# Performance work log

Measured on AMD Instinct MI355X. Metric: run time of the kernel, lower is better.

Reference implementation:

```python
import jax, jax.numpy as jnp
import numpy as np

DIM = 512
HEADS = 8
D_HEAD = 64
INNER_FF = 4 * DIM  # 2048
EPS = 1e-5
SCALE = D_HEAD ** -0.5


def _layernorm(x, w, b):
    x = x.astype(jnp.float32)
    mu = jnp.mean(x, axis=-1, keepdims=True)
    var = jnp.mean(jnp.square(x - mu), axis=-1, keepdims=True)
    return (x - mu) * jax.lax.rsqrt(var + EPS) * w + b


def _l2_attn(x, wq, bq, wv, bv, wo, bo):
    # x: [B, N, DIM]. k = q (context is ignored in the original module).
    b, n, _ = x.shape
    q = (x @ wq + bq).reshape(b, n, HEADS, D_HEAD).transpose(0, 2, 1, 3)  # b h n d
    v = (x @ wv + bv).reshape(b, n, HEADS, D_HEAD).transpose(0, 2, 1, 3)
    q = q.astype(jnp.float32)
    AB = jnp.einsum('bhid,bhjd->bhij', q, q)          # [b,h,n,n]
    AA = jnp.sum(jnp.square(q), axis=-1)               # [b,h,n]
    sim = -(AA[..., :, None] - 2.0 * AB + AA[..., None, :]) * SCALE
    attn = jax.nn.softmax(sim, axis=-1)
    out = jnp.einsum('bhij,bhjd->bhid', attn, v)       # [b,h,n,d]
    out = out.transpose(0, 2, 1, 3).reshape(b, n, HEADS * D_HEAD)
    return out @ wo + bo


def _geglu_ff(x, w1, b1, w2, b2):
    h = x @ w1 + b1                      # [B, N, 2*INNER_FF]
    a, gate = jnp.split(h, 2, axis=-1)
    return (a * jax.nn.gelu(gate, approximate=False)) @ w2 + b2


def setup_inputs() -> dict:
    key = jax.random.key(0)
    ks = jax.random.split(key, 24)
    s = 0.02
    d = {'x': jax.random.normal(ks[0], (4, 2048, DIM), jnp.float32)}
    # layernorms
    d['sa_norm_w'] = jnp.ones((DIM,), jnp.float32)
    d['sa_norm_b'] = jnp.zeros((DIM,), jnp.float32)
    d['ca_norm_w'] = jnp.ones((DIM,), jnp.float32)
    d['ca_norm_b'] = jnp.zeros((DIM,), jnp.float32)
    d['ff_norm_w'] = jnp.ones((DIM,), jnp.float32)
    d['ff_norm_b'] = jnp.zeros((DIM,), jnp.float32)
    # attn1 (self)
    d['a1_wq'] = jax.random.normal(ks[1], (DIM, DIM), jnp.float32) * s
    d['a1_bq'] = jnp.zeros((DIM,), jnp.float32)
    d['a1_wv'] = jax.random.normal(ks[2], (DIM, DIM), jnp.float32) * s
    d['a1_bv'] = jnp.zeros((DIM,), jnp.float32)
    d['a1_wo'] = jax.random.normal(ks[3], (DIM, DIM), jnp.float32) * s
    d['a1_bo'] = jnp.zeros((DIM,), jnp.float32)
    # attn2 (cross, but k=q and v from x in original code)
    d['a2_wq'] = jax.random.normal(ks[4], (DIM, DIM), jnp.float32) * s
    d['a2_bq'] = jnp.zeros((DIM,), jnp.float32)
    d['a2_wv'] = jax.random.normal(ks[5], (DIM, DIM), jnp.float32) * s
    d['a2_bv'] = jnp.zeros((DIM,), jnp.float32)
    d['a2_wo'] = jax.random.normal(ks[6], (DIM, DIM), jnp.float32) * s
    d['a2_bo'] = jnp.zeros((DIM,), jnp.float32)
    # GEGLU FFN
    d['ff_w1'] = jax.random.normal(ks[7], (DIM, 2 * INNER_FF), jnp.float32) * s
    d['ff_b1'] = jnp.zeros((2 * INNER_FF,), jnp.float32)
    d['ff_w2'] = jax.random.normal(ks[8], (INNER_FF, DIM), jnp.float32) * s
    d['ff_b2'] = jnp.zeros((DIM,), jnp.float32)
    return d


def reference(x, sa_norm_w, sa_norm_b, ca_norm_w, ca_norm_b, ff_norm_w, ff_norm_b,
              a1_wq, a1_bq, a1_wv, a1_bv, a1_wo, a1_bo,
              a2_wq, a2_bq, a2_wv, a2_bv, a2_wo, a2_bo,
              ff_w1, ff_b1, ff_w2, ff_b2):
    x = _l2_attn(_layernorm(x, sa_norm_w, sa_norm_b), a1_wq, a1_bq, a1_wv, a1_bv, a1_wo, a1_bo) + x
    x = _l2_attn(_layernorm(x, ca_norm_w, ca_norm_b), a2_wq, a2_bq, a2_wv, a2_bv, a2_wo, a2_bo) + x
    x = _geglu_ff(_layernorm(x, ff_norm_w, ff_norm_b), ff_w1, ff_b1, ff_w2, ff_b2) + x
    return x
```

## Files before the change

kernel.cpp:

```cpp
#include <hip/hip_runtime.h>
#include <hip/hip_bf16.h>


typedef short bf16x8 __attribute__((ext_vector_type(8)));
typedef float f32x4 __attribute__((ext_vector_type(4)));
typedef unsigned short u16;
typedef unsigned int u32;

__device__ __forceinline__ float bf2f(u16 u) {
    return __uint_as_float(((u32)u) << 16);
}
__device__ __forceinline__ u16 f2bf(float f) {
    u32 u = __float_as_uint(f);
    u32 rb = ((u >> 16) & 1u) + 0x7fffu;
    return (u16)((u + rb) >> 16);
}
__device__ __forceinline__ float gelu_fast(float x) {
    float y = 1.5957691216f * (x + 0.044715f * x * x * x);
    return x / (1.f + __expf(-y));
}
__device__ __forceinline__ void gl2lds16(const u16* g, u16* l) {
    __builtin_amdgcn_global_load_lds(
        (const __attribute__((address_space(1))) void*)(unsigned long long)(uintptr_t)g,
        (__attribute__((address_space(3))) void*)(unsigned long long)(uintptr_t)l,
        16, 0, 0);
}

struct TArgs {
    const float* src[8];
    u16* dst[8];
    int R[8], C[8];
    int start[9];
};
__global__ __launch_bounds__(256) void transpose_multi(TArgs a) {
    __shared__ float tile[32][33];
    int bid = blockIdx.x;
    int s = 0;
    while (bid >= a.start[s + 1]) s++;
    int local = bid - a.start[s];
    int R = a.R[s], C = a.C[s];
    int tx = C >> 5;
    int bx = local % tx, by = local / tx;
    const float* in = a.src[s];
    u16* out = a.dst[s];
    int t = threadIdx.x;
    int c = t & 31, r0 = (t >> 5) * 4;
#pragma unroll
    for (int i = 0; i < 4; i++)
        tile[r0 + i][c] = in[(size_t)(by * 32 + r0 + i) * C + bx * 32 + c];
    __syncthreads();
#pragma unroll
    for (int i = 0; i < 4; i++)
        out[(size_t)(bx * 32 + r0 + i) * R + by * 32 + c] = f2bf(tile[c][r0 + i]);
}

__global__ __launch_bounds__(256) void ln_kernel(const float* __restrict__ x,
                                                 const float* __restrict__ w,
                                                 const float* __restrict__ b,
                                                 u16* __restrict__ out) {
    int row = blockIdx.x, t = threadIdx.x;
    const float* xr = x + (size_t)row * 512;
    float2 v = *(const float2*)(xr + t * 2);
    float s1 = v.x + v.y;
    float s2 = v.x * v.x + v.y * v.y;
#pragma unroll
    for (int m = 1; m < 64; m <<= 1) {
        s1 += __shfl_xor(s1, m);
        s2 += __shfl_xor(s2, m);
    }
    __shared__ float r1[4], r2[4];
    int wave = t >> 6, lane = t & 63;
    if (lane == 0) { r1[wave] = s1; r2[wave] = s2; }
    __syncthreads();
    float tot1 = r1[0] + r1[1] + r1[2] + r1[3];
    float tot2 = r2[0] + r2[1] + r2[2] + r2[3];
    float mu = tot1 * (1.f / 512.f);
    float var = tot2 * (1.f / 512.f) - mu * mu;
    float rs = rsqrtf(var + 1e-5f);
    float2 wv = *(const float2*)(w + t * 2);
    float2 bv = *(const float2*)(b + t * 2);
    float o0 = (v.x - mu) * rs * wv.x + bv.x;
    float o1 = (v.y - mu) * rs * wv.y + bv.y;
    u32 pack = (u32)f2bf(o0) | ((u32)f2bf(o1) << 16);
    *(u32*)(out + (size_t)row * 512 + t * 2) = pack;
}

__global__ __launch_bounds__(256) void gemm_ff1(const u16* __restrict__ A,
                                                const u16* __restrict__ BT,
                                                const float* __restrict__ bias,
                                                u16* __restrict__ gout,
                                                int K) {
    __shared__ u16 As[2][128 * 32];
    __shared__ u16 Bs[2][128 * 32];
    int t = threadIdx.x;
    int wave = t >> 6, lane = t & 63, quad = lane >> 4, l16 = lane & 15;
    int m0 = blockIdx.x * 128, n0 = blockIdx.y * 64;
    f32x4 aacc[2][4], gacc[2][4];
#pragma unroll
    for (int i = 0; i < 2; i++)
#pragma unroll
        for (int j = 0; j < 4; j++) {
            aacc[i][j] = (f32x4){0.f, 0.f, 0.f, 0.f};
            gacc[i][j] = (f32x4){0.f, 0.f, 0.f, 0.f};
        }
    const u16* Ag = A + (size_t)(m0 + wave * 32 + (lane >> 2)) * K + (lane & 3) * 8;
    int brow = (wave < 2) ? (n0 + wave * 32) : (2048 + n0 + (wave - 2) * 32);
    const u16* Bg = BT + (size_t)(brow + (lane >> 2)) * K + (lane & 3) * 8;
    int lo = wave * 32 * 32;
    const size_t rstep = (size_t)16 * K;
    gl2lds16(Ag, &As[0][lo]);
    gl2lds16(Ag + rstep, &As[0][lo + 16 * 32]);
    gl2lds16(Bg, &Bs[0][lo]);
    gl2lds16(Bg + rstep, &Bs[0][lo + 16 * 32]);
    int buf = 0;
    for (int k0 = 0; k0 < K; k0 += 32, buf ^= 1) {
        int kn = (k0 + 32 < K) ? (k0 + 32) : k0;
        int nb = buf ^ 1;
        asm volatile("s_waitcnt lgkmcnt(0)\n\ts_barrier" ::: "memory");
        gl2lds16(Ag + kn, &As[nb][lo]);
        gl2lds16(Ag + kn + rstep, &As[nb][lo + 16 * 32]);
        gl2lds16(Bg + kn, &Bs[nb][lo]);
        gl2lds16(Bg + kn + rstep, &Bs[nb][lo + 16 * 32]);
        asm volatile("s_waitcnt vmcnt(4)\n\ts_barrier" ::: "memory");
        bf16x8 a[2];
#pragma unroll
        for (int i = 0; i < 2; i++)
            a[i] = *(const bf16x8*)&As[buf][(wave * 32 + i * 16 + l16) * 32 + quad * 8];
#pragma unroll
        for (int j = 0; j < 4; j++) {
            bf16x8 ba = *(const bf16x8*)&Bs[buf][(j * 16 + l16) * 32 + quad * 8];
            bf16x8 bg = *(const bf16x8*)&Bs[buf][(64 + j * 16 + l16) * 32 + quad * 8];
#pragma unroll
            for (int i = 0; i < 2; i++) {
                aacc[i][j] = __builtin_amdgcn_mfma_f32_16x16x32_bf16(a[i], ba, aacc[i][j], 0, 0, 0);
                gacc[i][j] = __builtin_amdgcn_mfma_f32_16x16x32_bf16(a[i], bg, gacc[i][j], 0, 0, 0);
            }
        }
    }
    asm volatile("s_waitcnt vmcnt(0)" ::: "memory");
    int row_base = m0 + wave * 32 + quad * 4;
#pragma unroll
    for (int j = 0; j < 4; j++) {
        int col = n0 + j * 16 + l16;
        float ba = bias[col];
        float bg = bias[2048 + col];
#pragma unroll
        for (int i = 0; i < 2; i++) {
#pragma unroll
            for (int r = 0; r < 4; r++) {
                int row = row_base + i * 16 + r;
                float av = aacc[i][j][r] + ba;
                float gv = gacc[i][j][r] + bg;
                gout[(size_t)row * 2048 + col] = f2bf(av * gelu_fast(gv));
            }
        }
    }
}

template <int MODE>
__global__ __launch_bounds__(256) void gemm_rect(const u16* __restrict__ A,
                                                 const u16* __restrict__ BT,
                                                 const float* __restrict__ bias,
                                                 const float* __restrict__ bias2,
                                                 const float* __restrict__ res,
                                                 float* __restrict__ outf,
                                                 u16* __restrict__ outb,
                                                 u16* __restrict__ outb2,
                                                 float* __restrict__ aa,
                                                 int M, int N, int K) {
    __shared__ u16 As[2][128 * 32];
    __shared__ u16 Bs[2][64 * 32];
    int t = threadIdx.x;
    int wave = t >> 6, lane = t & 63, quad = lane >> 4, l16 = lane & 15;
    int m0 = blockIdx.x * 128, n0 = blockIdx.y * 64;
    f32x4 acc[2][4];
#pragma unroll
    for (int i = 0; i < 2; i++)
#pragma unroll
        for (int j = 0; j < 4; j++) acc[i][j] = (f32x4){0.f, 0.f, 0.f, 0.f};
    const u16* Ag = A + (size_t)(m0 + wave * 32 + (lane >> 2)) * K + (lane & 3) * 8;
    const u16* Bg = BT + (size_t)(n0 + wave * 16 + (lane >> 2)) * K + (lane & 3) * 8;
    int loA = wave * 32 * 32;
    int loB = wave * 16 * 32;
    const size_t rstep = (size_t)16 * K;
    gl2lds16(Ag, &As[0][loA]);
    gl2lds16(Ag + rstep, &As[0][loA + 16 * 32]);
    gl2lds16(Bg, &Bs[0][loB]);
    int buf = 0;
    for (int k0 = 0; k0 < K; k0 += 32, buf ^= 1) {
        int kn = (k0 + 32 < K) ? (k0 + 32) : k0;
        int nb = buf ^ 1;
        asm volatile("s_waitcnt lgkmcnt(0)\n\ts_barrier" ::: "memory");
        gl2lds16(Ag + kn, &As[nb][loA]);
        gl2lds16(Ag + kn + rstep, &As[nb][loA + 16 * 32]);
        gl2lds16(Bg + kn, &Bs[nb][loB]);
        asm volatile("s_waitcnt vmcnt(3)\n\ts_barrier" ::: "memory");
        bf16x8 a[2], b[4];
#pragma unroll
        for (int i = 0; i < 2; i++)
            a[i] = *(const bf16x8*)&As[buf][(wave * 32 + i * 16 + l16) * 32 + quad * 8];
#pragma unroll
        for (int j = 0; j < 4; j++)
            b[j] = *(const bf16x8*)&Bs[buf][(j * 16 + l16) * 32 + quad * 8];
#pragma unroll
        for (int i = 0; i < 2; i++)
#pragma unroll
            for (int j = 0; j < 4; j++)
                acc[i][j] = __builtin_amdgcn_mfma_f32_16x16x32_bf16(a[i], b[j], acc[i][j], 0, 0, 0);
    }
    asm volatile("s_waitcnt vmcnt(0)" ::: "memory");
    int row_base = m0 + wave * 32 + quad * 4;
    float ssq[2][4];
#pragma unroll
    for (int i = 0; i < 2; i++)
#pragma unroll
        for (int r = 0; r < 4; r++) ssq[i][r] = 0.f;
#pragma unroll
    for (int j = 0; j < 4; j++) {
        int col = n0 + j * 16 + l16;
        float bv;
        if (MODE == 4) bv = (col < 512) ? bias[col] : bias2[col - 512];
        else bv = bias[col];
#pragma unroll
        for (int i = 0; i < 2; i++) {
            int rowA = row_base + i * 16;
            if (MODE == 4) {
                if (col < 512) {
                    int hh = col >> 6, d = col & 63;
#pragma unroll
                    for (int r = 0; r < 4; r++) {
                        int row = rowA + r;
                        float v = acc[i][j][r] + bv;
                        ssq[i][r] += v * v;
                        outb[((size_t)((row >> 11) * 8 + hh) * 2048 + (row & 2047)) * 64 + d] = f2bf(v);
                    }
                } else {
                    int c2 = col - 512;
                    int hh = c2 >> 6, d = c2 & 63;
                    int n = rowA & 2047;
                    int a4 = (n >> 2) & 7;
                    int ncol = (n & ~31) + ((a4 & 3) << 3) + ((a4 >> 2) << 2);
                    u32 plo = (u32)f2bf(acc[i][j][0] + bv) | ((u32)f2bf(acc[i][j][1] + bv) << 16);
                    u32 phi = (u32)f2bf(acc[i][j][2] + bv) | ((u32)f2bf(acc[i][j][3] + bv) << 16);
                    uint2 pk; pk.x = plo; pk.y = phi;
                    *(uint2*)&outb2[((size_t)((rowA >> 11) * 8 + hh) * 64 + d) * 2048 + ncol] = pk;
                }
            } else {
#pragma unroll
                for (int r = 0; r < 4; r++) {
                    size_t idx = (size_t)(rowA + r) * N + col;
                    outf[idx] = acc[i][j][r] + bv + res[idx];
                }
            }
        }
    }
    if (MODE == 4 && n0 < 512) {
        int hh = n0 >> 6;
#pragma unroll
        for (int i = 0; i < 2; i++) {
#pragma unroll
            for (int r = 0; r < 4; r++) {
                float s = ssq[i][r];
                s += __shfl_xor(s, 1); s += __shfl_xor(s, 2);
                s += __shfl_xor(s, 4); s += __shfl_xor(s, 8);
                if (l16 == 0) {
                    int row = row_base + i * 16 + r;
                    aa[(size_t)((row >> 11) * 8 + hh) * 2048 + (row & 2047)] = s * 0.125f;
                }
            }
        }
    }
}

__global__ __launch_bounds__(256) void attn_mfma(const u16* __restrict__ qbuf,
                                                 const u16* __restrict__ vtp,
                                                 const float* __restrict__ aas,
                                                 u16* __restrict__ out) {
    __shared__ u16 Qj[64][72];
    __shared__ u16 VT[64][72];
    int bid = blockIdx.x;
    int bh = bid & 31;
    int itile = bid >> 5;
    const u16* qb = qbuf + (size_t)bh * 2048 * 64;
    const u16* vtb = vtp + (size_t)bh * 64 * 2048;
    const float* aab = aas + (size_t)bh * 2048;
    int t = threadIdx.x;
    int wave = t >> 6, lane = t & 63, quad = lane >> 4, l16 = lane & 15;
    int ibase = itile * 64 + wave * 16;
    bf16x8 qf0 = *(const bf16x8*)(qb + (size_t)(ibase + l16) * 64 + quad * 8);
    bf16x8 qf1 = *(const bf16x8*)(qb + (size_t)(ibase + l16) * 64 + 32 + quad * 8);
    float ci = aab[ibase + l16];
    f32x4 O[4];
#pragma unroll
    for (int nt = 0; nt < 4; nt++) O[nt] = (f32x4){0.f, 0.f, 0.f, 0.f};
    float lr = 0.f;
    int sr = t >> 2, sc = (t & 3) * 16;
    uint4 nq0, nq1, nv0, nv1;
    {
        const u16* srcq = qb + (size_t)sr * 64 + sc;
        nq0 = *(const uint4*)srcq;
        nq1 = *(const uint4*)(srcq + 8);
        const u16* srcv = vtb + (size_t)sr * 2048 + sc;
        nv0 = *(const uint4*)srcv;
        nv1 = *(const uint4*)(srcv + 8);
    }
    for (int j0 = 0; j0 < 2048; j0 += 64) {
        __syncthreads();
        *(uint4*)&Qj[sr][sc] = nq0;
        *(uint4*)&Qj[sr][sc + 8] = nq1;
        *(uint4*)&VT[sr][sc] = nv0;
        *(uint4*)&VT[sr][sc + 8] = nv1;
        if (j0 + 64 < 2048) {
            const u16* srcq = qb + (size_t)(j0 + 64 + sr) * 64 + sc;
            nq0 = *(const uint4*)srcq;
            nq1 = *(const uint4*)(srcq + 8);
            const u16* srcv = vtb + (size_t)sr * 2048 + (j0 + 64) + sc;
            nv0 = *(const uint4*)srcv;
            nv1 = *(const uint4*)(srcv + 8);
        }
        __syncthreads();
#pragma unroll
        for (int c = 0; c < 2; c++) {
            int j1 = c * 32, j2 = c * 32 + 16;
            bf16x8 a10 = *(const bf16x8*)&Qj[j1 + l16][quad * 8];
            bf16x8 a11 = *(const bf16x8*)&Qj[j1 + l16][32 + quad * 8];
            f32x4 s0 = {0.f, 0.f, 0.f, 0.f};
            s0 = __builtin_amdgcn_mfma_f32_16x16x32_bf16(a10, qf0, s0, 0, 0, 0);
            s0 = __builtin_amdgcn_mfma_f32_16x16x32_bf16(a11, qf1, s0, 0, 0, 0);
            bf16x8 a20 = *(const bf16x8*)&Qj[j2 + l16][quad * 8];
            bf16x8 a21 = *(const bf16x8*)&Qj[j2 + l16][32 + quad * 8];
            f32x4 s1 = {0.f, 0.f, 0.f, 0.f};
            s1 = __builtin_amdgcn_mfma_f32_16x16x32_bf16(a20, qf0, s1, 0, 0, 0);
            s1 = __builtin_amdgcn_mfma_f32_16x16x32_bf16(a21, qf1, s1, 0, 0, 0);
            float4 aav0 = *(const float4*)(aab + j0 + j1 + quad * 4);
            float4 aav1 = *(const float4*)(aab + j0 + j2 + quad * 4);
            float p0 = __expf(s0[0] * 0.25f - aav0.x - ci);
            float p1 = __expf(s0[1] * 0.25f - aav0.y - ci);
            float p2 = __expf(s0[2] * 0.25f - aav0.z - ci);
            float p3 = __expf(s0[3] * 0.25f - aav0.w - ci);
            float p4 = __expf(s1[0] * 0.25f - aav1.x - ci);
            float p5 = __expf(s1[1] * 0.25f - aav1.y - ci);
            float p6 = __expf(s1[2] * 0.25f - aav1.z - ci);
            float p7 = __expf(s1[3] * 0.25f - aav1.w - ci);
            lr += (p0 + p1 + p2 + p3) + (p4 + p5 + p6 + p7);
            bf16x8 pa;
            u32* pu = (u32*)&pa;
            pu[0] = __builtin_amdgcn_perm(__float_as_uint(p1), __float_as_uint(p0), 0x07060302u);
            pu[1] = __builtin_amdgcn_perm(__float_as_uint(p3), __float_as_uint(p2), 0x07060302u);
            pu[2] = __builtin_amdgcn_perm(__float_as_uint(p5), __float_as_uint(p4), 0x07060302u);
            pu[3] = __builtin_amdgcn_perm(__float_as_uint(p7), __float_as_uint(p6), 0x07060302u);
#pragma unroll
            for (int nt = 0; nt < 4; nt++) {
                bf16x8 vf = *(const bf16x8*)&VT[nt * 16 + l16][c * 32 + quad * 8];
                O[nt] = __builtin_amdgcn_mfma_f32_16x16x32_bf16(pa, vf, O[nt], 0, 0, 0);
            }
        }
    }
    lr += __shfl_xor(lr, 16);
    lr += __shfl_xor(lr, 32);
    float inv = 1.f / lr;
    int b = bh >> 3, h = bh & 7;
#pragma unroll
    for (int r = 0; r < 4; r++) {
        float invr = __shfl(inv, quad * 4 + r);
        size_t row = (size_t)(b * 2048 + ibase + quad * 4 + r);
        u16* o = out + row * 512 + h * 64 + l16;
        o[0]  = f2bf(O[0][r] * invr);
        o[16] = f2bf(O[1][r] * invr);
        o[32] = f2bf(O[2][r] * invr);
        o[48] = f2bf(O[3][r] * invr);
    }
}

extern "C" void kernel_launch(void* const* d_in, const int* in_sizes, int n_in,
                              void* d_out, int out_size, void* d_ws, size_t ws_size,
                              hipStream_t stream) {
    const float* x      = (const float*)d_in[0];
    const float* sa_w   = (const float*)d_in[1];
    const float* sa_b   = (const float*)d_in[2];
    const float* ca_w   = (const float*)d_in[3];
    const float* ca_b   = (const float*)d_in[4];
    const float* ffn_w  = (const float*)d_in[5];
    const float* ffn_b  = (const float*)d_in[6];
    const float* a1_wq  = (const float*)d_in[7];
    const float* a1_bq  = (const float*)d_in[8];
    const float* a1_wv  = (const float*)d_in[9];
    const float* a1_bv  = (const float*)d_in[10];
    const float* a1_wo  = (const float*)d_in[11];
    const float* a1_bo  = (const float*)d_in[12];
    const float* a2_wq  = (const float*)d_in[13];
    const float* a2_bq  = (const float*)d_in[14];
    const float* a2_wv  = (const float*)d_in[15];
    const float* a2_bv  = (const float*)d_in[16];
    const float* a2_wo  = (const float*)d_in[17];
    const float* a2_bo  = (const float*)d_in[18];
    const float* ff_w1  = (const float*)d_in[19];
    const float* ff_b1  = (const float*)d_in[20];
    const float* ff_w2  = (const float*)d_in[21];
    const float* ff_b2  = (const float*)d_in[22];

    char* ws = (char*)d_ws;
    const size_t MB = 1ull << 20;
    float* x_res   = (float*)(ws);
    u16* xn        = (u16*)(ws + 16 * MB);
    u16* wT_a1qv   = (u16*)(ws + 24 * MB);
    u16* wT_a2qv   = (u16*)(ws + 25 * MB);
    u16* wT_a1o    = (u16*)(ws + 26 * MB);
    u16* wT_a2o    = (u16*)(ws + 26 * MB + 512 * 1024);
    u16* wT_ff1    = (u16*)(ws + 27 * MB);
    u16* wT_ff2    = (u16*)(ws + 31 * MB);
    u16* qbuf      = (u16*)(ws + 34 * MB);
    u16* vtp       = (u16*)(ws + 42 * MB);
    float* aab     = (float*)(ws + 50 * MB);
    u16* attn_o    = (u16*)(ws + 51 * MB);
    u16* gbuf      = (u16*)(ws + 60 * MB);

    (void)in_sizes; (void)n_in; (void)out_size; (void)ws_size;

    TArgs ta;
    ta.src[0] = a1_wq; ta.dst[0] = wT_a1qv;               ta.R[0] = 512;  ta.C[0] = 512;
    ta.src[1] = a1_wv; ta.dst[1] = wT_a1qv + 512 * 512;   ta.R[1] = 512;  ta.C[1] = 512;
    ta.src[2] = a2_wq; ta.dst[2] = wT_a2qv;               ta.R[2] = 512;  ta.C[2] = 512;
    ta.src[3] = a2_wv; ta.dst[3] = wT_a2qv + 512 * 512;   ta.R[3] = 512;  ta.C[3] = 512;
    ta.src[4] = a1_wo; ta.dst[4] = wT_a1o;                ta.R[4] = 512;  ta.C[4] = 512;
    ta.src[5] = a2_wo; ta.dst[5] = wT_a2o;                ta.R[5] = 512;  ta.C[5] = 512;
    ta.src[6] = ff_w1; ta.dst[6] = wT_ff1;                ta.R[6] = 512;  ta.C[6] = 4096;
    ta.src[7] = ff_w2; ta.dst[7] = wT_ff2;                ta.R[7] = 2048; ta.C[7] = 512;
    ta.start[0] = 0;
    for (int s = 0; s < 8; s++)
        ta.start[s + 1] = ta.start[s] + (ta.C[s] >> 5) * (ta.R[s] >> 5);
    transpose_multi<<<ta.start[8], 256, 0, stream>>>(ta);

    ln_kernel<<<8192, 256, 0, stream>>>(x, sa_w, sa_b, xn);
    gemm_rect<4><<<dim3(64, 16), 256, 0, stream>>>(xn, wT_a1qv, a1_bq, a1_bv, nullptr, nullptr, qbuf, vtp, aab, 8192, 1024, 512);
    attn_mfma<<<1024, 256, 0, stream>>>(qbuf, vtp, aab, attn_o);
    gemm_rect<2><<<dim3(64, 8), 256, 0, stream>>>(attn_o, wT_a1o, a1_bo, nullptr, x, x_res, nullptr, nullptr, nullptr, 8192, 512, 512);

    ln_kernel<<<8192, 256, 0, stream>>>(x_res, ca_w, ca_b, xn);
    gemm_rect<4><<<dim3(64, 16), 256, 0, stream>>>(xn, wT_a2qv, a2_bq, a2_bv, nullptr, nullptr, qbuf, vtp, aab, 8192, 1024, 512);
    attn_mfma<<<1024, 256, 0, stream>>>(qbuf, vtp, aab, attn_o);
    gemm_rect<2><<<dim3(64, 8), 256, 0, stream>>>(attn_o, wT_a2o, a2_bo, nullptr, x_res, x_res, nullptr, nullptr, nullptr, 8192, 512, 512);

    ln_kernel<<<8192, 256, 0, stream>>>(x_res, ffn_w, ffn_b, xn);
    gemm_ff1<<<dim3(64, 32), 256, 0, stream>>>(xn, wT_ff1, ff_b1, gbuf, 512);
    gemm_rect<2><<<dim3(64, 8), 256, 0, stream>>>(gbuf, wT_ff2, ff_b2, nullptr, x_res, (float*)d_out, nullptr, nullptr, nullptr, 8192, 512, 2048);
}
```

Measured before the change: 413.4 us.

## Split attention key range in two with partial outputs and combine kernel

The attention kernel now splits the 2048-key loop into two halves, doubling the grid to 2048 blocks. Each block writes unnormalized fp32 partial outputs and row sums to workspace. A new combine kernel adds the halves, normalizes and writes bf16. This works without max-rescaling because the softmax uses a fixed offset, not a running max. MFMA sections are also wrapped in s_setprio to favour matrix issue. The split buys more parallelism at the cost of an extra launch and fp32 partial traffic.

```diff
diff --git a/kernel.cpp b/kernel.cpp
--- a/kernel.cpp
+++ b/kernel.cpp
@@ -275,12 +275,15 @@
 __global__ __launch_bounds__(256) void attn_mfma(const u16* __restrict__ qbuf,
                                                  const u16* __restrict__ vtp,
                                                  const float* __restrict__ aas,
-                                                 u16* __restrict__ out) {
+                                                 float* __restrict__ opart,
+                                                 float* __restrict__ lrpart) {
     __shared__ u16 Qj[64][72];
     __shared__ u16 VT[64][72];
     int bid = blockIdx.x;
     int bh = bid & 31;
-    int itile = bid >> 5;
+    int jsplit = (bid >> 5) & 1;
+    int itile = bid >> 6;
+    int jbase = jsplit << 10;
     const u16* qb = qbuf + (size_t)bh * 2048 * 64;
     const u16* vtb = vtp + (size_t)bh * 64 * 2048;
     const float* aab = aas + (size_t)bh * 2048;
@@ -297,20 +300,20 @@
     int sr = t >> 2, sc = (t & 3) * 16;
     uint4 nq0, nq1, nv0, nv1;
     {
-        const u16* srcq = qb + (size_t)sr * 64 + sc;
+        const u16* srcq = qb + (size_t)(jbase + sr) * 64 + sc;
         nq0 = *(const uint4*)srcq;
         nq1 = *(const uint4*)(srcq + 8);
-        const u16* srcv = vtb + (size_t)sr * 2048 + sc;
+        const u16* srcv = vtb + (size_t)sr * 2048 + jbase + sc;
         nv0 = *(const uint4*)srcv;
         nv1 = *(const uint4*)(srcv + 8);
     }
-    for (int j0 = 0; j0 < 2048; j0 += 64) {
+    for (int j0 = jbase; j0 < jbase + 1024; j0 += 64) {
         __syncthreads();
         *(uint4*)&Qj[sr][sc] = nq0;
         *(uint4*)&Qj[sr][sc + 8] = nq1;
         *(uint4*)&VT[sr][sc] = nv0;
         *(uint4*)&VT[sr][sc + 8] = nv1;
-        if (j0 + 64 < 2048) {
+        if (j0 + 64 < jbase + 1024) {
             const u16* srcq = qb + (size_t)(j0 + 64 + sr) * 64 + sc;
             nq0 = *(const uint4*)srcq;
             nq1 = *(const uint4*)(srcq + 8);
@@ -324,14 +327,16 @@
             int j1 = c * 32, j2 = c * 32 + 16;
             bf16x8 a10 = *(const bf16x8*)&Qj[j1 + l16][quad * 8];
             bf16x8 a11 = *(const bf16x8*)&Qj[j1 + l16][32 + quad * 8];
+            bf16x8 a20 = *(const bf16x8*)&Qj[j2 + l16][quad * 8];
+            bf16x8 a21 = *(const bf16x8*)&Qj[j2 + l16][32 + quad * 8];
+            __builtin_amdgcn_s_setprio(1);
             f32x4 s0 = {0.f, 0.f, 0.f, 0.f};
             s0 = __builtin_amdgcn_mfma_f32_16x16x32_bf16(a10, qf0, s0, 0, 0, 0);
             s0 = __builtin_amdgcn_mfma_f32_16x16x32_bf16(a11, qf1, s0, 0, 0, 0);
-            bf16x8 a20 = *(const bf16x8*)&Qj[j2 + l16][quad * 8];
-            bf16x8 a21 = *(const bf16x8*)&Qj[j2 + l16][32 + quad * 8];
             f32x4 s1 = {0.f, 0.f, 0.f, 0.f};
             s1 = __builtin_amdgcn_mfma_f32_16x16x32_bf16(a20, qf0, s1, 0, 0, 0);
             s1 = __builtin_amdgcn_mfma_f32_16x16x32_bf16(a21, qf1, s1, 0, 0, 0);
+            __builtin_amdgcn_s_setprio(0);
             float4 aav0 = *(const float4*)(aab + j0 + j1 + quad * 4);
             float4 aav1 = *(const float4*)(aab + j0 + j2 + quad * 4);
             float p0 = __expf(s0[0] * 0.25f - aav0.x - ci);
@@ -349,27 +354,59 @@
             pu[1] = __builtin_amdgcn_perm(__float_as_uint(p3), __float_as_uint(p2), 0x07060302u);
             pu[2] = __builtin_amdgcn_perm(__float_as_uint(p5), __float_as_uint(p4), 0x07060302u);
             pu[3] = __builtin_amdgcn_perm(__float_as_uint(p7), __float_as_uint(p6), 0x07060302u);
+            __builtin_amdgcn_s_setprio(1);
 #pragma unroll
             for (int nt = 0; nt < 4; nt++) {
                 bf16x8 vf = *(const bf16x8*)&VT[nt * 16 + l16][c * 32 + quad * 8];
                 O[nt] = __builtin_amdgcn_mfma_f32_16x16x32_bf16(pa, vf, O[nt], 0, 0, 0);
             }
+            __builtin_amdgcn_s_setprio(0);
         }
     }
     lr += __shfl_xor(lr, 16);
     lr += __shfl_xor(lr, 32);
+    size_t pslot = (size_t)jsplit * 32 + bh;
+    if (lane < 16)
+        lrpart[pslot * 2048 + ibase + l16] = lr;
+    float* ob = opart + (pslot * 2048 + ibase + quad * 4) * 64 + l16;
+#pragma unroll
+    for (int r = 0; r < 4; r++) {
+        float* o = ob + (size_t)r * 64;
+        o[0]  = O[0][r];
+        o[16] = O[1][r];
+        o[32] = O[2][r];
+        o[48] = O[3][r];
+    }
+}
+
+__global__ __launch_bounds__(256) void attn_combine(const float* __restrict__ opart,
+                                                    const float* __restrict__ lrpart,
+                                                    u16* __restrict__ out) {
+    int t = threadIdx.x;
+    int rl = t >> 3, d0 = (t & 7) * 8;
+    int rg = blockIdx.x * 32 + rl;
+    int bh = rg >> 11, i = rg & 2047;
+    const float* o0 = opart + ((size_t)bh * 2048 + i) * 64 + d0;
+    const float* o1 = o0 + (size_t)32 * 2048 * 64;
+    float lr = lrpart[(size_t)bh * 2048 + i] +
+               lrpart[(size_t)32 * 2048 + (size_t)bh * 2048 + i];
     float inv = 1.f / lr;
+    float4 a0 = *(const float4*)o0;
+    float4 a1 = *(const float4*)(o0 + 4);
+    float4 b0 = *(const float4*)o1;
+    float4 b1 = *(const float4*)(o1 + 4);
     int b = bh >> 3, h = bh & 7;
-#pragma unroll
-    for (int r = 0; r < 4; r++) {
-        float invr = __shfl(inv, quad * 4 + r);
-        size_t row = (size_t)(b * 2048 + ibase + quad * 4 + r);
-        u16* o = out + row * 512 + h * 64 + l16;
-        o[0]  = f2bf(O[0][r] * invr);
-        o[16] = f2bf(O[1][r] * invr);
-        o[32] = f2bf(O[2][r] * invr);
-        o[48] = f2bf(O[3][r] * invr);
-    }
+    u16* op = out + ((size_t)(b * 2048 + i)) * 512 + h * 64 + d0;
+    u16 r[8];
+    r[0] = f2bf((a0.x + b0.x) * inv);
+    r[1] = f2bf((a0.y + b0.y) * inv);
+    r[2] = f2bf((a0.z + b0.z) * inv);
+    r[3] = f2bf((a0.w + b0.w) * inv);
+    r[4] = f2bf((a1.x + b1.x) * inv);
+    r[5] = f2bf((a1.y + b1.y) * inv);
+    r[6] = f2bf((a1.z + b1.z) * inv);
+    r[7] = f2bf((a1.w + b1.w) * inv);
+    *(uint4*)op = *(uint4*)r;
 }
 
 extern "C" void kernel_launch(void* const* d_in, const int* in_sizes, int n_in,
@@ -412,8 +449,10 @@
     u16* qbuf      = (u16*)(ws + 34 * MB);
     u16* vtp       = (u16*)(ws + 42 * MB);
     float* aab     = (float*)(ws + 50 * MB);
+    float* lrp     = (float*)(ws + 50 * MB + 256 * 1024);
     u16* attn_o    = (u16*)(ws + 51 * MB);
     u16* gbuf      = (u16*)(ws + 60 * MB);
+    float* opart   = (float*)(ws + 60 * MB);
 
     (void)in_sizes; (void)n_in; (void)out_size; (void)ws_size;
 
@@ -433,12 +472,14 @@
 
     ln_kernel<<<8192, 256, 0, stream>>>(x, sa_w, sa_b, xn);
     gemm_rect<4><<<dim3(64, 16), 256, 0, stream>>>(xn, wT_a1qv, a1_bq, a1_bv, nullptr, nullptr, qbuf, vtp, aab, 8192, 1024, 512);
-    attn_mfma<<<1024, 256, 0, stream>>>(qbuf, vtp, aab, attn_o);
+    attn_mfma<<<2048, 256, 0, stream>>>(qbuf, vtp, aab, opart, lrp);
+    attn_combine<<<2048, 256, 0, stream>>>(opart, lrp, attn_o);
     gemm_rect<2><<<dim3(64, 8), 256, 0, stream>>>(attn_o, wT_a1o, a1_bo, nullptr, x, x_res, nullptr, nullptr, nullptr, 8192, 512, 512);
 
     ln_kernel<<<8192, 256, 0, stream>>>(x_res, ca_w, ca_b, xn);
     gemm_rect<4><<<dim3(64, 16), 256, 0, stream>>>(xn, wT_a2qv, a2_bq, a2_bv, nullptr, nullptr, qbuf, vtp, aab, 8192, 1024, 512);
-    attn_mfma<<<1024, 256, 0, stream>>>(qbuf, vtp, aab, attn_o);
+    attn_mfma<<<2048, 256, 0, stream>>>(qbuf, vtp, aab, opart, lrp);
+    attn_combine<<<2048, 256, 0, stream>>>(opart, lrp, attn_o);
     gemm_rect<2><<<dim3(64, 8), 256, 0, stream>>>(attn_o, wT_a2o, a2_bo, nullptr, x_res, x_res, nullptr, nullptr, nullptr, 8192, 512, 512);
 
     ln_kernel<<<8192, 256, 0, stream>>>(x_res, ffn_w, ffn_b, xn);
```

Measured after the change: 429.6 us. +3.9%, slower.

## Double-buffer attention tiles with XOR-swizzled LDS and two query subtiles per wave

Applied to the files above, without the earlier changes.

The attention kernel now has each wave process 32 query rows (two 16-row subtiles), so every K/V fragment loaded from LDS feeds twice as many MFMAs. The block count is halved to match. LDS is double-buffered with a single barrier per iteration, and a row-XOR swizzle replaces the padded layout to avoid bank conflicts. s_setprio hints are wrapped around the MFMA sections. The cost is higher register pressure and fewer blocks (512 across the CUs), which may reduce occupancy and latency hiding.

```diff
diff --git a/kernel.cpp b/kernel.cpp
--- a/kernel.cpp
+++ b/kernel.cpp
@@ -276,8 +276,7 @@
                                                  const u16* __restrict__ vtp,
                                                  const float* __restrict__ aas,
                                                  u16* __restrict__ out) {
-    __shared__ u16 Qj[64][72];
-    __shared__ u16 VT[64][72];
+    __shared__ u16 L[2][8192];
     int bid = blockIdx.x;
     int bh = bid & 31;
     int itile = bid >> 5;
@@ -286,89 +285,128 @@
     const float* aab = aas + (size_t)bh * 2048;
     int t = threadIdx.x;
     int wave = t >> 6, lane = t & 63, quad = lane >> 4, l16 = lane & 15;
-    int ibase = itile * 64 + wave * 16;
-    bf16x8 qf0 = *(const bf16x8*)(qb + (size_t)(ibase + l16) * 64 + quad * 8);
-    bf16x8 qf1 = *(const bf16x8*)(qb + (size_t)(ibase + l16) * 64 + 32 + quad * 8);
-    float ci = aab[ibase + l16];
-    f32x4 O[4];
-#pragma unroll
-    for (int nt = 0; nt < 4; nt++) O[nt] = (f32x4){0.f, 0.f, 0.f, 0.f};
-    float lr = 0.f;
-    int sr = t >> 2, sc = (t & 3) * 16;
-    uint4 nq0, nq1, nv0, nv1;
+    int ibase = itile * 128 + wave * 32;
+    int sw = l16 & 7;
+
+    bf16x8 qf[2][2];
+    float ci[2];
+    f32x4 O[2][4];
+    float lr[2] = {0.f, 0.f};
+#pragma unroll
+    for (int st = 0; st < 2; st++) {
+        const u16* qr = qb + (size_t)(ibase + st * 16 + l16) * 64;
+        qf[st][0] = *(const bf16x8*)(qr + quad * 8);
+        qf[st][1] = *(const bf16x8*)(qr + 32 + quad * 8);
+        ci[st] = aab[ibase + st * 16 + l16];
+#pragma unroll
+        for (int nt = 0; nt < 4; nt++) O[st][nt] = (f32x4){0.f, 0.f, 0.f, 0.f};
+    }
+
+    int r1 = t >> 3, cs = t & 7;
+    int wof1 = r1 * 64 + 8 * (cs ^ (r1 & 7));
+    int wof2 = (r1 + 32) * 64 + 8 * (cs ^ (r1 & 7));
+
     {
-        const u16* srcq = qb + (size_t)sr * 64 + sc;
-        nq0 = *(const uint4*)srcq;
-        nq1 = *(const uint4*)(srcq + 8);
-        const u16* srcv = vtb + (size_t)sr * 2048 + sc;
-        nv0 = *(const uint4*)srcv;
-        nv1 = *(const uint4*)(srcv + 8);
-    }
-    for (int j0 = 0; j0 < 2048; j0 += 64) {
+        uint4 pq1 = *(const uint4*)(qb + (size_t)r1 * 64 + cs * 8);
+        uint4 pq2 = *(const uint4*)(qb + (size_t)(r1 + 32) * 64 + cs * 8);
+        uint4 pv1 = *(const uint4*)(vtb + (size_t)r1 * 2048 + cs * 8);
+        uint4 pv2 = *(const uint4*)(vtb + (size_t)(r1 + 32) * 2048 + cs * 8);
+        *(uint4*)&L[0][wof1] = pq1;
+        *(uint4*)&L[0][wof2] = pq2;
+        *(uint4*)&L[0][4096 + wof1] = pv1;
+        *(uint4*)&L[0][4096 + wof2] = pv2;
+    }
+    __syncthreads();
+
+    for (int it = 0; it < 32; ++it) {
+        int cur = it & 1;
+        int j0 = it << 6;
+        uint4 pq1, pq2, pv1, pv2;
+        bool more = (it + 1 < 32);
+        if (more) {
+            int j0n = j0 + 64;
+            pq1 = *(const uint4*)(qb + (size_t)(j0n + r1) * 64 + cs * 8);
+            pq2 = *(const uint4*)(qb + (size_t)(j0n + r1 + 32) * 64 + cs * 8);
+            pv1 = *(const uint4*)(vtb + (size_t)r1 * 2048 + j0n + cs * 8);
+            pv2 = *(const uint4*)(vtb + (size_t)(r1 + 32) * 2048 + j0n + cs * 8);
+        }
+        const u16* Q = &L[cur][0];
+        const u16* V = &L[cur][4096];
+#pragma unroll
+        for (int c = 0; c < 2; c++) {
+            int r10 = c * 32 + l16, r20 = c * 32 + 16 + l16;
+            bf16x8 a10 = *(const bf16x8*)&Q[r10 * 64 + 8 * (quad ^ sw)];
+            bf16x8 a11 = *(const bf16x8*)&Q[r10 * 64 + 8 * ((4 + quad) ^ sw)];
+            bf16x8 a20 = *(const bf16x8*)&Q[r20 * 64 + 8 * (quad ^ sw)];
+            bf16x8 a21 = *(const bf16x8*)&Q[r20 * 64 + 8 * ((4 + quad) ^ sw)];
+            f32x4 s0[2], s1[2];
+            __builtin_amdgcn_s_setprio(1);
+#pragma unroll
+            for (int st = 0; st < 2; st++) {
+                f32x4 z = {0.f, 0.f, 0.f, 0.f};
+                s0[st] = __builtin_amdgcn_mfma_f32_16x16x32_bf16(a10, qf[st][0], z, 0, 0, 0);
+                s0[st] = __builtin_amdgcn_mfma_f32_16x16x32_bf16(a11, qf[st][1], s0[st], 0, 0, 0);
+                s1[st] = __builtin_amdgcn_mfma_f32_16x16x32_bf16(a20, qf[st][0], z, 0, 0, 0);
+                s1[st] = __builtin_amdgcn_mfma_f32_16x16x32_bf16(a21, qf[st][1], s1[st], 0, 0, 0);
+            }
+            __builtin_amdgcn_s_setprio(0);
+            float4 aav0 = *(const float4*)(aab + j0 + c * 32 + quad * 4);
+            float4 aav1 = *(const float4*)(aab + j0 + c * 32 + 16 + quad * 4);
+            bf16x8 pa[2];
+#pragma unroll
+            for (int st = 0; st < 2; st++) {
+                float p0 = __expf(s0[st][0] * 0.25f - aav0.x - ci[st]);
+                float p1 = __expf(s0[st][1] * 0.25f - aav0.y - ci[st]);
+                float p2 = __expf(s0[st][2] * 0.25f - aav0.z - ci[st]);
+                float p3 = __expf(s0[st][3] * 0.25f - aav0.w - ci[st]);
+                float p4 = __expf(s1[st][0] * 0.25f - aav1.x - ci[st]);
+                float p5 = __expf(s1[st][1] * 0.25f - aav1.y - ci[st]);
+                float p6 = __expf(s1[st][2] * 0.25f - aav1.z - ci[st]);
+                float p7 = __expf(s1[st][3] * 0.25f - aav1.w - ci[st]);
+                lr[st] += (p0 + p1 + p2 + p3) + (p4 + p5 + p6 + p7);
+                u32* pu = (u32*)&pa[st];
+                pu[0] = __builtin_amdgcn_perm(__float_as_uint(p1), __float_as_uint(p0), 0x07060302u);
+                pu[1] = __builtin_amdgcn_perm(__float_as_uint(p3), __float_as_uint(p2), 0x07060302u);
+                pu[2] = __builtin_amdgcn_perm(__float_as_uint(p5), __float_as_uint(p4), 0x07060302u);
+                pu[3] = __builtin_amdgcn_perm(__float_as_uint(p7), __float_as_uint(p6), 0x07060302u);
+            }
+            __builtin_amdgcn_s_setprio(1);
+#pragma unroll
+            for (int nt = 0; nt < 4; nt++) {
+                int rv = nt * 16 + l16;
+                bf16x8 vf = *(const bf16x8*)&V[rv * 64 + 8 * ((c * 4 + quad) ^ sw)];
+                O[0][nt] = __builtin_amdgcn_mfma_f32_16x16x32_bf16(pa[0], vf, O[0][nt], 0, 0, 0);
+                O[1][nt] = __builtin_amdgcn_mfma_f32_16x16x32_bf16(pa[1], vf, O[1][nt], 0, 0, 0);
+            }
+            __builtin_amdgcn_s_setprio(0);
+        }
+        if (more) {
+            u16* D = &L[cur ^ 1][0];
+            *(uint4*)&D[wof1] = pq1;
+            *(uint4*)&D[wof2] = pq2;
+            *(uint4*)&D[4096 + wof1] = pv1;
+            *(uint4*)&D[4096 + wof2] = pv2;
+        }
         __syncthreads();
-        *(uint4*)&Qj[sr][sc] = nq0;
-        *(uint4*)&Qj[sr][sc + 8] = nq1;
-        *(uint4*)&VT[sr][sc] = nv0;
-        *(uint4*)&VT[sr][sc + 8] = nv1;
-        if (j0 + 64 < 2048) {
-            const u16* srcq = qb + (size_t)(j0 + 64 + sr) * 64 + sc;
-            nq0 = *(const uint4*)srcq;
-            nq1 = *(const uint4*)(srcq + 8);
-            const u16* srcv = vtb + (size_t)sr * 2048 + (j0 + 64) + sc;
-            nv0 = *(const uint4*)srcv;
-            nv1 = *(const uint4*)(srcv + 8);
-        }
-        __syncthreads();
-#pragma unroll
-        for (int c = 0; c < 2; c++) {
-            int j1 = c * 32, j2 = c * 32 + 16;
-            bf16x8 a10 = *(const bf16x8*)&Qj[j1 + l16][quad * 8];
-            bf16x8 a11 = *(const bf16x8*)&Qj[j1 + l16][32 + quad * 8];
-            f32x4 s0 = {0.f, 0.f, 0.f, 0.f};
-            s0 = __builtin_amdgcn_mfma_f32_16x16x32_bf16(a10, qf0, s0, 0, 0, 0);
-            s0 = __builtin_amdgcn_mfma_f32_16x16x32_bf16(a11, qf1, s0, 0, 0, 0);
-            bf16x8 a20 = *(const bf16x8*)&Qj[j2 + l16][quad * 8];
-            bf16x8 a21 = *(const bf16x8*)&Qj[j2 + l16][32 + quad * 8];
-            f32x4 s1 = {0.f, 0.f, 0.f, 0.f};
-            s1 = __builtin_amdgcn_mfma_f32_16x16x32_bf16(a20, qf0, s1, 0, 0, 0);
-            s1 = __builtin_amdgcn_mfma_f32_16x16x32_bf16(a21, qf1, s1, 0, 0, 0);
-            float4 aav0 = *(const float4*)(aab + j0 + j1 + quad * 4);
-            float4 aav1 = *(const float4*)(aab + j0 + j2 + quad * 4);
-            float p0 = __expf(s0[0] * 0.25f - aav0.x - ci);
-            float p1 = __expf(s0[1] * 0.25f - aav0.y - ci);
-            float p2 = __expf(s0[2] * 0.25f - aav0.z - ci);
-            float p3 = __expf(s0[3] * 0.25f - aav0.w - ci);
-            float p4 = __expf(s1[0] * 0.25f - aav1.x - ci);
-            float p5 = __expf(s1[1] * 0.25f - aav1.y - ci);
-            float p6 = __expf(s1[2] * 0.25f - aav1.z - ci);
-            float p7 = __expf(s1[3] * 0.25f - aav1.w - ci);
-            lr += (p0 + p1 + p2 + p3) + (p4 + p5 + p6 + p7);
-            bf16x8 pa;
-            u32* pu = (u32*)&pa;
-            pu[0] = __builtin_amdgcn_perm(__float_as_uint(p1), __float_as_uint(p0), 0x07060302u);
-            pu[1] = __builtin_amdgcn_perm(__float_as_uint(p3), __float_as_uint(p2), 0x07060302u);
-            pu[2] = __builtin_amdgcn_perm(__float_as_uint(p5), __float_as_uint(p4), 0x07060302u);
-            pu[3] = __builtin_amdgcn_perm(__float_as_uint(p7), __float_as_uint(p6), 0x07060302u);
-#pragma unroll
-            for (int nt = 0; nt < 4; nt++) {
-                bf16x8 vf = *(const bf16x8*)&VT[nt * 16 + l16][c * 32 + quad * 8];
-                O[nt] = __builtin_amdgcn_mfma_f32_16x16x32_bf16(pa, vf, O[nt], 0, 0, 0);
-            }
-        }
-    }
-    lr += __shfl_xor(lr, 16);
-    lr += __shfl_xor(lr, 32);
-    float inv = 1.f / lr;
+    }
+
     int b = bh >> 3, h = bh & 7;
 #pragma unroll
-    for (int r = 0; r < 4; r++) {
-        float invr = __shfl(inv, quad * 4 + r);
-        size_t row = (size_t)(b * 2048 + ibase + quad * 4 + r);
-        u16* o = out + row * 512 + h * 64 + l16;
-        o[0]  = f2bf(O[0][r] * invr);
-        o[16] = f2bf(O[1][r] * invr);
-        o[32] = f2bf(O[2][r] * invr);
-        o[48] = f2bf(O[3][r] * invr);
+    for (int st = 0; st < 2; st++) {
+        float l = lr[st];
+        l += __shfl_xor(l, 16);
+        l += __shfl_xor(l, 32);
+        float inv = 1.f / l;
+#pragma unroll
+        for (int r = 0; r < 4; r++) {
+            float invr = __shfl(inv, quad * 4 + r);
+            size_t row = (size_t)(b * 2048 + ibase + st * 16 + quad * 4 + r);
+            u16* o = out + row * 512 + h * 64 + l16;
+            o[0]  = f2bf(O[st][0][r] * invr);
+            o[16] = f2bf(O[st][1][r] * invr);
+            o[32] = f2bf(O[st][2][r] * invr);
+            o[48] = f2bf(O[st][3][r] * invr);
+        }
     }
 }
 
@@ -433,12 +471,12 @@
 
     ln_kernel<<<8192, 256, 0, stream>>>(x, sa_w, sa_b, xn);
     gemm_rect<4><<<dim3(64, 16), 256, 0, stream>>>(xn, wT_a1qv, a1_bq, a1_bv, nullptr, nullptr, qbuf, vtp, aab, 8192, 1024, 512);
-    attn_mfma<<<1024, 256, 0, stream>>>(qbuf, vtp, aab, attn_o);
+    attn_mfma<<<512, 256, 0, stream>>>(qbuf, vtp, aab, attn_o);
     gemm_rect<2><<<dim3(64, 8), 256, 0, stream>>>(attn_o, wT_a1o, a1_bo, nullptr, x, x_res, nullptr, nullptr, nullptr, 8192, 512, 512);
 
     ln_kernel<<<8192, 256, 0, stream>>>(x_res, ca_w, ca_b, xn);
     gemm_rect<4><<<dim3(64, 16), 256, 0, stream>>>(xn, wT_a2qv, a2_bq, a2_bv, nullptr, nullptr, qbuf, vtp, aab, 8192, 1024, 512);
-    attn_mfma<<<1024, 256, 0, stream>>>(qbuf, vtp, aab, attn_o);
+    attn_mfma<<<512, 256, 0, stream>>>(qbuf, vtp, aab, attn_o);
     gemm_rect<2><<<dim3(64, 8), 256, 0, stream>>>(attn_o, wT_a2o, a2_bo, nullptr, x_res, x_res, nullptr, nullptr, nullptr, 8192, 512, 512);
 
     ln_kernel<<<8192, 256, 0, stream>>>(x_res, ffn_w, ffn_b, xn);
```

After: 384.9 us. 1.07x faster.
